# Kernel optimization log

Measured on AMD Instinct MI355X. Metric: run time of the kernel, lower is better.

The kernel has to match this reference:

```python
import jax, jax.numpy as jnp
import numpy as np

B, T, M, P, N2 = 16, 8192, 128, 128, 128  # N2 = N//2 complex modes

def setup_inputs() -> dict:
    key = jax.random.key(0)
    k1, k2, k3, k4, k5 = jax.random.split(key, 5)
    u = jax.random.normal(k1, (B, T, M), dtype=jnp.float32)
    # log-parametrized Lambda (S5 'log' convention): Lambda = -exp(row0) + 1j*row1
    log_re = jnp.log(jax.random.uniform(k2, (N2,), minval=0.1, maxval=1.0))
    im = jnp.pi * jnp.arange(N2, dtype=jnp.float32)  # HiPPO-like imaginary spread
    Lambda_param = jnp.stack([log_re, im], axis=0).astype(jnp.float32)
    B_param = jax.random.normal(k3, (2, N2, M), dtype=jnp.float32) / np.sqrt(M)
    C_param = jax.random.normal(k4, (2, P, N2), dtype=jnp.float32) / np.sqrt(N2)
    delta = jnp.array([0.01], dtype=jnp.float32)  # default_\u0394
    return {"u": u, "Lambda_param": Lambda_param, "B_param": B_param,
            "C_param": C_param, "delta": delta}

def reference(u, Lambda_param, B_param, C_param, delta):
    # Reconstruct complex continuous-time matrices
    Lam = (-jnp.exp(Lambda_param[0]) + 1j * Lambda_param[1]).astype(jnp.complex64)   # (N2,)
    Bc = (B_param[0] + 1j * B_param[1]).astype(jnp.complex64)                        # (N2, M)
    Cc = (C_param[0] + 1j * C_param[1]).astype(jnp.complex64)                        # (P, N2)
    d = delta[0]
    # ZOH discretization: Lambda_d = exp(Lam*d), Bd = ((Lambda_d - 1)/Lam) * B
    Ld = jnp.exp(Lam * d)                                                            # (N2,)
    Bd = ((Ld - 1.0) / Lam)[:, None] * Bc                                            # (N2, M)
    # Input projection: Bu[b,t,n] = sum_m u[b,t,m] * Bd[n,m]
    Bu = jnp.einsum('btm,nm->btn', u.astype(jnp.complex64), Bd)                      # (B,T,N2)
    # Parallel scan of x_{k+1} = Ld * x_k + Bu_k, x_0 = 0 -> x holds x_1..x_T
    A = jnp.broadcast_to(Ld, Bu.shape)
    def comb(e1, e2):
        a1, b1 = e1
        a2, b2 = e2
        return (a1 * a2, a2 * b1 + b2)
    _, x = jax.lax.associative_scan(comb, (A, Bu), axis=1)                           # (B,T,N2)
    # return_next_y=True: y_k = 2*Re(C x_{k+1})
    y = 2.0 * jnp.real(jnp.einsum('btn,pn->btp', x, Cc))                             # (B,T,P)
    return y
```

## Files before the change

### kernel.cpp

```cpp
#include <hip/hip_runtime.h>
#include <hip/hip_bf16.h>

#define LCH 128
#define NCH 64
#define NCHUNKS 1024

typedef __attribute__((ext_vector_type(8))) short short8v;
typedef __attribute__((ext_vector_type(4))) short short4v;
typedef __attribute__((ext_vector_type(4))) float f32x4;

#define W2_LDINV 0
#define W2_LDP   16384
#define W2_E     32768
#define W2_CIN   163840
#define WS_WPACK_BYTE  2359296
#define WS_CCPACK_BYTE (2359296 + 65536)
#define WS_BUS_BYTE    (2359296 + 131072)
#define WS_NEED ((size_t)WS_BUS_BYTE + (size_t)NCHUNKS * 65536)

#define BUS_BYTE(s, np) ((((s) >> 3) * 4096) + ((np) * 16) + (((s) & 7) * 2))

__device__ inline unsigned short f2bf(float f) {
    union { __hip_bfloat16 h; unsigned short u; } v;
    v.h = __float2bfloat16(f);
    return v.u;
}
__device__ inline short4v pack4(float a, float b, float c, float d) {
    union { __hip_bfloat162 h2[2]; short4v s4; } pk;
    pk.h2[0] = __float22bfloat162_rn(make_float2(a, b));
    pk.h2[1] = __float22bfloat162_rn(make_float2(c, d));
    return pk.s4;
}

__global__ void k0_all(const float* __restrict__ lp, const float* __restrict__ bp,
                       const float* __restrict__ cp, const float* __restrict__ delta,
                       float2* __restrict__ ws2, unsigned short* __restrict__ wpack,
                       unsigned short* __restrict__ ccpack) {
    const int r = blockIdx.x;
    const int tid = threadIdx.x;
    if (r < 128) {
        if (tid < 256) {
            const int n = tid & 127;
            const double d = (double)delta[0];
            const double lre = -exp((double)lp[n]);
            const double lim = (double)lp[128 + n];
            const double kk = (double)(r + 1) * d;
            if (tid < 128) {
                const double mag = exp(-lre * kk);
                ws2[W2_LDINV + r * 128 + n] = make_float2((float)(mag * cos(lim * kk)),
                                                          (float)(-mag * sin(lim * kk)));
            } else {
                const double mag = exp(lre * kk);
                ws2[W2_LDP + r * 128 + n] = make_float2((float)(mag * cos(lim * kk)),
                                                        (float)(mag * sin(lim * kk)));
            }
        }
    } else if (r < 192) {
        const int gid = (r - 128) * 512 + tid;
        const int j = gid & 7;
        const int lane = (gid >> 3) & 63;
        const int ks = (gid >> 9) & 3;
        const int ntile = gid >> 11;
        const int np = ntile * 16 + (lane & 15);
        const int m = ks * 32 + ((lane >> 4) & 3) * 8 + j;
        const int n = np & 127;
        const double d = (double)delta[0];
        const double lre = -exp((double)lp[n]);
        const double lim = (double)lp[128 + n];
        const double er = exp(lre * d);
        const double ldr = er * cos(lim * d), ldi = er * sin(lim * d);
        const double nr = ldr - 1.0, ni = ldi;
        const double den = lre * lre + lim * lim;
        const double cr = (nr * lre + ni * lim) / den;
        const double ci = (ni * lre - nr * lim) / den;
        const double br = (double)bp[n * 128 + m];
        const double bi = (double)bp[16384 + n * 128 + m];
        const double v = (np < 128) ? (cr * br - ci * bi) : (cr * bi + ci * br);
        wpack[gid] = f2bf((float)v);
    } else {
        const int gid = (r - 192) * 512 + tid;
        const int j = gid & 7;
        const int lane = (gid >> 3) & 63;
        const int ks = (gid >> 9) & 7;
        const int ptile = gid >> 12;
        const int p = ptile * 16 + (lane & 15);
        const int k = ks * 32 + ((lane >> 4) & 3) * 8 + j;
        const int n = k >> 1;
        const float v = ((k & 1) == 0) ? 2.0f * cp[p * 128 + n]
                                       : -2.0f * cp[16384 + p * 128 + n];
        ccpack[gid] = f2bf(v);
    }
}

__device__ inline void stage_u(const float* __restrict__ uchunk, unsigned short* lds_u) {
    const float4* uf = (const float4*)uchunk;
    const int tid = threadIdx.x;
#pragma unroll
    for (int it = 0; it < 8; ++it) {
        const int f4 = it * 512 + tid;
        const float4 v = uf[f4];
        const int t = f4 >> 5;
        const int m = (f4 & 31) * 4;
        const int byte = (t * 256 + m * 2) ^ ((t & 7) << 4);
        *(short4v*)((char*)lds_u + byte) = pack4(v.x, v.y, v.z, v.w);
    }
}

__global__ __launch_bounds__(512, 4) void k3a_bus(const float* __restrict__ u,
                                                  float2* __restrict__ ws2,
                                                  const unsigned short* __restrict__ wpack,
                                                  char* __restrict__ busg) {
    __shared__ unsigned short lds_u[16384];
    const int tid = threadIdx.x;
    const int lane = tid & 63;
    const int w = tid >> 6;
    const int tl = lane & 15;
    const int gq = (lane >> 4) & 3;
    const int g = blockIdx.x;
    const int b = g >> 6;
    const int c = g & 63;
    const int n = w * 16 + tl;
    const short8v* wp = (const short8v*)wpack;
    char* busc = busg + (size_t)g * 65536;
    const float4* uf = (const float4*)(u + (size_t)(b * 8192 + c * 128) * 128);

    {
        float4 p0 = uf[tid], p1 = uf[512 + tid], p2 = uf[1024 + tid], p3 = uf[1536 + tid];
#pragma unroll
        for (int it = 0; it < 4; ++it) {
            const float4 v = (it == 0) ? p0 : (it == 1) ? p1 : (it == 2) ? p2 : p3;
            const int f4 = it * 512 + tid;
            const int t = f4 >> 5;
            const int m = (f4 & 31) * 4;
            const int byte = (t * 256 + m * 2) ^ ((t & 7) << 4);
            *(short4v*)((char*)lds_u + byte) = pack4(v.x, v.y, v.z, v.w);
        }
    }
    float4 q0 = uf[2048 + tid], q1 = uf[2560 + tid], q2 = uf[3072 + tid], q3 = uf[3584 + tid];
    __builtin_amdgcn_sched_barrier(0);
    __syncthreads();

    float er = 0.f, ei = 0.f;

    {
        f32x4 acc[4][2];
#pragma unroll
        for (int i = 0; i < 4; ++i) { acc[i][0] = (f32x4)0.f; acc[i][1] = (f32x4)0.f; }
        __builtin_amdgcn_s_setprio(1);
#pragma unroll
        for (int ks = 0; ks < 4; ++ks) {
            const short8v b0 = wp[(w * 4 + ks) * 64 + lane];
            const short8v b1 = wp[((8 + w) * 4 + ks) * 64 + lane];
#pragma unroll
            for (int tt2 = 0; tt2 < 4; ++tt2) {
                const int t = tt2 * 16 + tl;
                const int byte = (t * 256 + (ks * 32 + gq * 8) * 2) ^ ((t & 7) << 4);
                const short8v a = *(const short8v*)((const char*)lds_u + byte);
                acc[tt2][0] = __builtin_amdgcn_mfma_f32_16x16x32_bf16(a, b0, acc[tt2][0], 0, 0, 0);
                acc[tt2][1] = __builtin_amdgcn_mfma_f32_16x16x32_bf16(a, b1, acc[tt2][1], 0, 0, 0);
            }
        }
        __builtin_amdgcn_s_setprio(0);
#pragma unroll
        for (int tt2 = 0; tt2 < 4; ++tt2) {
            float vr[4], vi[4];
#pragma unroll
            for (int reg = 0; reg < 4; ++reg) {
                const int rr = tt2 * 16 + gq * 4 + reg;
                const float2 li = ws2[W2_LDINV + rr * 128 + n];
                const float br = acc[tt2][0][reg], bi = acc[tt2][1][reg];
                vr[reg] = li.x * br - li.y * bi;
                vi[reg] = li.x * bi + li.y * br;
                er += vr[reg];
                ei += vi[reg];
            }
            const int s0 = tt2 * 16 + gq * 4;
            const int rowr = w * 16 + tl;
            const int rowi = 128 + rowr;
            *(short4v*)(busc + BUS_BYTE(s0, rowr)) = pack4(vr[0], vr[1], vr[2], vr[3]);
            *(short4v*)(busc + BUS_BYTE(s0, rowi)) = pack4(vi[0], vi[1], vi[2], vi[3]);
        }
    }

    {
#pragma unroll
        for (int it = 0; it < 4; ++it) {
            const float4 v = (it == 0) ? q0 : (it == 1) ? q1 : (it == 2) ? q2 : q3;
            const int f4 = 2048 + it * 512 + tid;
            const int t = f4 >> 5;
            const int m = (f4 & 31) * 4;
            const int byte = (t * 256 + m * 2) ^ ((t & 7) << 4);
            *(short4v*)((char*)lds_u + byte) = pack4(v.x, v.y, v.z, v.w);
        }
    }
    __syncthreads();

    {
        f32x4 acc[4][2];
#pragma unroll
        for (int i = 0; i < 4; ++i) { acc[i][0] = (f32x4)0.f; acc[i][1] = (f32x4)0.f; }
        __builtin_amdgcn_s_setprio(1);
#pragma unroll
        for (int ks = 0; ks < 4; ++ks) {
            const short8v b0 = wp[(w * 4 + ks) * 64 + lane];
            const short8v b1 = wp[((8 + w) * 4 + ks) * 64 + lane];
#pragma unroll
            for (int tt2 = 0; tt2 < 4; ++tt2) {
                const int t = (4 + tt2) * 16 + tl;
                const int byte = (t * 256 + (ks * 32 + gq * 8) * 2) ^ ((t & 7) << 4);
                const short8v a = *(const short8v*)((const char*)lds_u + byte);
                acc[tt2][0] = __builtin_amdgcn_mfma_f32_16x16x32_bf16(a, b0, acc[tt2][0], 0, 0, 0);
                acc[tt2][1] = __builtin_amdgcn_mfma_f32_16x16x32_bf16(a, b1, acc[tt2][1], 0, 0, 0);
            }
        }
        __builtin_amdgcn_s_setprio(0);
#pragma unroll
        for (int tt2 = 0; tt2 < 4; ++tt2) {
            float vr[4], vi[4];
#pragma unroll
            for (int reg = 0; reg < 4; ++reg) {
                const int rr = (4 + tt2) * 16 + gq * 4 + reg;
                const float2 li = ws2[W2_LDINV + rr * 128 + n];
                const float br = acc[tt2][0][reg], bi = acc[tt2][1][reg];
                vr[reg] = li.x * br - li.y * bi;
                vi[reg] = li.x * bi + li.y * br;
                er += vr[reg];
                ei += vi[reg];
            }
            const int s0 = (4 + tt2) * 16 + gq * 4;
            const int rowr = w * 16 + tl;
            const int rowi = 128 + rowr;
            *(short4v*)(busc + BUS_BYTE(s0, rowr)) = pack4(vr[0], vr[1], vr[2], vr[3]);
            *(short4v*)(busc + BUS_BYTE(s0, rowi)) = pack4(vi[0], vi[1], vi[2], vi[3]);
        }
    }

    er += __shfl_xor(er, 16); ei += __shfl_xor(ei, 16);
    er += __shfl_xor(er, 32); ei += __shfl_xor(ei, 32);
    const float2 ld = ws2[W2_LDP + 127 * 128 + n];
    if (lane < 16) {
        ws2[W2_E + g * 128 + n] = make_float2(ld.x * er - ld.y * ei,
                                              ld.x * ei + ld.y * er);
    }
}

__global__ void k2_carry(float2* __restrict__ ws2) {
    const int idx = blockIdx.x * 256 + threadIdx.x;
    const int b = idx >> 7;
    const int n = idx & 127;
    const float2 l = ws2[W2_LDP + 127 * 128 + n];
    float cr = 0.f, ci = 0.f;
    for (int c = 0; c < NCH; ++c) {
        const int o = (b * NCH + c) * 128 + n;
        ws2[W2_CIN + o] = make_float2(cr, ci);
        const float2 e = ws2[W2_E + o];
        const float nr = fmaf(l.x, cr, fmaf(-l.y, ci, e.x));
        const float ni = fmaf(l.x, ci, fmaf(l.y, cr, e.y));
        cr = nr; ci = ni;
    }
}

__global__ __launch_bounds__(512, 6) void k3b_out(const float2* __restrict__ ws2,
                                                  const char* __restrict__ busg,
                                                  const unsigned short* __restrict__ ccpack,
                                                  float* __restrict__ y) {
    __shared__ unsigned short lds[32768];
    const int tid = threadIdx.x;
    const int lane = tid & 63;
    const int w = tid >> 6;
    const int tl = lane & 15;
    const int gq = (lane >> 4) & 3;
    const int g = blockIdx.x;
    const int b = g >> 6;
    const int c = g & 63;
    const int n = w * 16 + tl;
    const short8v* cc8 = (const short8v*)ccpack;
    const char* busc = busg + (size_t)g * 65536;

    short8v ONES, D0, D1;
#pragma unroll
    for (int j = 0; j < 8; ++j) {
        const int sl = gq * 8 + j;
        ONES[j] = (short)0x3F80;
        D0[j] = (sl <= tl) ? (short)0x3F80 : (short)0;
        D1[j] = (sl <= tl + 16) ? (short)0x3F80 : (short)0;
    }
    const float2 cin = ws2[W2_CIN + g * 128 + n];
    const int rowr = w * 16 + tl;
    const int rowi = 128 + rowr;

    {
        f32x4 z[4][2];
#pragma unroll
        for (int i = 0; i < 4; ++i) { z[i][0] = (f32x4)0.f; z[i][1] = (f32x4)0.f; }
        __builtin_amdgcn_s_setprio(1);
#pragma unroll
        for (int ks = 0; ks < 2; ++ks) {
            const int sb = ks * 32 + gq * 8;
            const short8v b0 = *(const short8v*)(busc + BUS_BYTE(sb, rowr));
            const short8v b1 = *(const short8v*)(busc + BUS_BYTE(sb, rowi));
#pragma unroll
            for (int tt = 0; tt < 4; ++tt) {
                if (tt < 2 * ks) continue;
                const short8v a = (tt == 2 * ks) ? D0 : ((tt == 2 * ks + 1) ? D1 : ONES);
                z[tt][0] = __builtin_amdgcn_mfma_f32_16x16x32_bf16(a, b0, z[tt][0], 0, 0, 0);
                z[tt][1] = __builtin_amdgcn_mfma_f32_16x16x32_bf16(a, b1, z[tt][1], 0, 0, 0);
            }
        }
        __builtin_amdgcn_s_setprio(0);
#pragma unroll
        for (int tt = 0; tt < 4; ++tt) {
#pragma unroll
            for (int reg = 0; reg < 4; ++reg) {
                const int r = tt * 16 + gq * 4 + reg;
                const float2 ld = ws2[W2_LDP + r * 128 + n];
                const float zr = z[tt][0][reg] + cin.x;
                const float zi = z[tt][1][reg] + cin.y;
                const float xr = ld.x * zr - ld.y * zi;
                const float xi = ld.x * zi + ld.y * zr;
                union { __hip_bfloat162 h2; unsigned uu; } pk;
                pk.h2 = __float22bfloat162_rn(make_float2(xr, xi));
                const int byte = (r * 512 + n * 4) ^ ((r & 7) << 4);
                *(unsigned*)((char*)lds + byte) = pk.uu;
            }
        }
    }

    {
        f32x4 z[4][2];
#pragma unroll
        for (int i = 0; i < 4; ++i) { z[i][0] = (f32x4)0.f; z[i][1] = (f32x4)0.f; }
        __builtin_amdgcn_s_setprio(1);
#pragma unroll
        for (int ks = 0; ks < 4; ++ks) {
            const int sb = ks * 32 + gq * 8;
            const short8v b0 = *(const short8v*)(busc + BUS_BYTE(sb, rowr));
            const short8v b1 = *(const short8v*)(busc + BUS_BYTE(sb, rowi));
#pragma unroll
            for (int tt2 = 0; tt2 < 4; ++tt2) {
                const int tt = 4 + tt2;
                if (tt < 2 * ks) continue;
                const short8v a = (tt == 2 * ks) ? D0 : ((tt == 2 * ks + 1) ? D1 : ONES);
                z[tt2][0] = __builtin_amdgcn_mfma_f32_16x16x32_bf16(a, b0, z[tt2][0], 0, 0, 0);
                z[tt2][1] = __builtin_amdgcn_mfma_f32_16x16x32_bf16(a, b1, z[tt2][1], 0, 0, 0);
            }
        }
        __builtin_amdgcn_s_setprio(0);
#pragma unroll
        for (int tt2 = 0; tt2 < 4; ++tt2) {
#pragma unroll
            for (int reg = 0; reg < 4; ++reg) {
                const int r = (4 + tt2) * 16 + gq * 4 + reg;
                const float2 ld = ws2[W2_LDP + r * 128 + n];
                const float zr = z[tt2][0][reg] + cin.x;
                const float zi = z[tt2][1][reg] + cin.y;
                const float xr = ld.x * zr - ld.y * zi;
                const float xi = ld.x * zi + ld.y * zr;
                union { __hip_bfloat162 h2; unsigned uu; } pk;
                pk.h2 = __float22bfloat162_rn(make_float2(xr, xi));
                const int byte = (r * 512 + n * 4) ^ ((r & 7) << 4);
                *(unsigned*)((char*)lds + byte) = pk.uu;
            }
        }
    }
    __syncthreads();

    f32x4 yac[8];
#pragma unroll
    for (int i = 0; i < 8; ++i) yac[i] = (f32x4)0.f;
    __builtin_amdgcn_s_setprio(1);
#pragma unroll
    for (int ks = 0; ks < 8; ++ks) {
        const short8v bfrg = cc8[(w * 8 + ks) * 64 + lane];
#pragma unroll
        for (int tt = 0; tt < 8; ++tt) {
            const int t = tt * 16 + tl;
            const int byte = (t * 512 + (ks * 32 + gq * 8) * 2) ^ ((t & 7) << 4);
            const short8v a = *(const short8v*)((const char*)lds + byte);
            yac[tt] = __builtin_amdgcn_mfma_f32_16x16x32_bf16(a, bfrg, yac[tt], 0, 0, 0);
        }
    }
    __builtin_amdgcn_s_setprio(0);
    const int p = w * 16 + tl;
    float* yrow = y + (size_t)(b * 8192 + c * 128) * 128;
#pragma unroll
    for (int tt = 0; tt < 8; ++tt) {
#pragma unroll
        for (int reg = 0; reg < 4; ++reg) {
            const int t = tt * 16 + gq * 4 + reg;
            yrow[t * 128 + p] = yac[tt][reg];
        }
    }
}

__global__ __launch_bounds__(512, 4) void k1_end(const float* __restrict__ u,
                                                 float2* __restrict__ ws2,
                                                 const unsigned short* __restrict__ wpack) {
    __shared__ unsigned short lds_u[16384];
    const int tid = threadIdx.x;
    const int lane = tid & 63;
    const int w = tid >> 6;
    const int tl = lane & 15;
    const int gq = (lane >> 4) & 3;
    const int g = blockIdx.x;
    const int b = g >> 6;
    const int c = g & 63;
    const int n = w * 16 + tl;
    stage_u(u + (size_t)(b * 8192 + c * 128) * 128, lds_u);
    __syncthreads();
    const short8v* wp = (const short8v*)wpack;
    float er = 0.f, ei = 0.f;
#pragma unroll
    for (int h = 0; h < 2; ++h) {
        f32x4 acc[4][2];
#pragma unroll
        for (int i = 0; i < 4; ++i) { acc[i][0] = (f32x4)0.f; acc[i][1] = (f32x4)0.f; }
        __builtin_amdgcn_s_setprio(1);
#pragma unroll
        for (int ks = 0; ks < 4; ++ks) {
            const short8v b0 = wp[(w * 4 + ks) * 64 + lane];
            const short8v b1 = wp[((8 + w) * 4 + ks) * 64 + lane];
#pragma unroll
            for (int tt2 = 0; tt2 < 4; ++tt2) {
                const int t = (h * 4 + tt2) * 16 + tl;
                const int byte = (t * 256 + (ks * 32 + gq * 8) * 2) ^ ((t & 7) << 4);
                const short8v a = *(const short8v*)((const char*)lds_u + byte);
                acc[tt2][0] = __builtin_amdgcn_mfma_f32_16x16x32_bf16(a, b0, acc[tt2][0], 0, 0, 0);
                acc[tt2][1] = __builtin_amdgcn_mfma_f32_16x16x32_bf16(a, b1, acc[tt2][1], 0, 0, 0);
            }
        }
        __builtin_amdgcn_s_setprio(0);
        __builtin_amdgcn_sched_barrier(0);
#pragma unroll
        for (int tt2 = 0; tt2 < 4; ++tt2) {
#pragma unroll
            for (int reg = 0; reg < 4; ++reg) {
                const int r = (h * 4 + tt2) * 16 + gq * 4 + reg;
                const float2 li = ws2[W2_LDINV + r * 128 + n];
                const float br = acc[tt2][0][reg], bi = acc[tt2][1][reg];
                er += li.x * br - li.y * bi;
                ei += li.x * bi + li.y * br;
            }
        }
        __builtin_amdgcn_sched_barrier(0);
    }
    er += __shfl_xor(er, 16); ei += __shfl_xor(ei, 16);
    er += __shfl_xor(er, 32); ei += __shfl_xor(ei, 32);
    const float2 ld = ws2[W2_LDP + 127 * 128 + n];
    if (lane < 16) {
        ws2[W2_E + g * 128 + n] = make_float2(ld.x * er - ld.y * ei,
                                              ld.x * ei + ld.y * er);
    }
}

__global__ __launch_bounds__(512, 4) void k3_main(const float* __restrict__ u,
                                                  const float2* __restrict__ ws2,
                                                  const unsigned short* __restrict__ wpack,
                                                  const unsigned short* __restrict__ ccpack,
                                                  float* __restrict__ y) {
    __shared__ unsigned short lds[32768];
    const int tid = threadIdx.x;
    const int lane = tid & 63;
    const int w = tid >> 6;
    const int tl = lane & 15;
    const int gq = (lane >> 4) & 3;
    const int g = blockIdx.x;
    const int b = g >> 6;
    const int c = g & 63;
    const int n = w * 16 + tl;
    const short8v* wp = (const short8v*)wpack;
    const short8v* cc8 = (const short8v*)ccpack;

    stage_u(u + (size_t)(b * 8192 + c * 128) * 128, lds);
    __syncthreads();
#pragma unroll
    for (int hh = 0; hh < 2; ++hh) {
        const int h = 1 - hh;
        f32x4 acc[4][2];
#pragma unroll
        for (int i = 0; i < 4; ++i) { acc[i][0] = (f32x4)0.f; acc[i][1] = (f32x4)0.f; }
        __builtin_amdgcn_s_setprio(1);
#pragma unroll
        for (int ks = 0; ks < 4; ++ks) {
            const short8v b0 = wp[(w * 4 + ks) * 64 + lane];
            const short8v b1 = wp[((8 + w) * 4 + ks) * 64 + lane];
#pragma unroll
            for (int tt2 = 0; tt2 < 4; ++tt2) {
                const int t = (h * 4 + tt2) * 16 + tl;
                const int byte = (t * 256 + (ks * 32 + gq * 8) * 2) ^ ((t & 7) << 4);
                const short8v a = *(const short8v*)((const char*)lds + byte);
                acc[tt2][0] = __builtin_amdgcn_mfma_f32_16x16x32_bf16(a, b0, acc[tt2][0], 0, 0, 0);
                acc[tt2][1] = __builtin_amdgcn_mfma_f32_16x16x32_bf16(a, b1, acc[tt2][1], 0, 0, 0);
            }
        }
        __builtin_amdgcn_s_setprio(0);
        __builtin_amdgcn_sched_barrier(0);
        if (h == 0) __syncthreads();
#pragma unroll
        for (int tt2 = 0; tt2 < 4; ++tt2) {
            float vr[4], vi[4];
#pragma unroll
            for (int reg = 0; reg < 4; ++reg) {
                const int r = (h * 4 + tt2) * 16 + gq * 4 + reg;
                const float2 li = ws2[W2_LDINV + r * 128 + n];
                const float br = acc[tt2][0][reg], bi = acc[tt2][1][reg];
                vr[reg] = li.x * br - li.y * bi;
                vi[reg] = li.x * bi + li.y * br;
            }
            const int s0 = (h * 4 + tt2) * 16 + gq * 4;
            const int rowr = w * 16 + tl;
            const int rowi = 128 + rowr;
            *(short4v*)((char*)lds + BUS_BYTE(s0, rowr)) = pack4(vr[0], vr[1], vr[2], vr[3]);
            *(short4v*)((char*)lds + BUS_BYTE(s0, rowi)) = pack4(vi[0], vi[1], vi[2], vi[3]);
        }
        __builtin_amdgcn_sched_barrier(0);
    }
    short8v ONES, D0, D1;
#pragma unroll
    for (int j = 0; j < 8; ++j) {
        const int sl = gq * 8 + j;
        ONES[j] = (short)0x3F80;
        D0[j] = (sl <= tl) ? (short)0x3F80 : (short)0;
        D1[j] = (sl <= tl + 16) ? (short)0x3F80 : (short)0;
    }
    f32x4 z[8][2];
#pragma unroll
    for (int i = 0; i < 8; ++i) { z[i][0] = (f32x4)0.f; z[i][1] = (f32x4)0.f; }
#pragma unroll
    for (int ks = 0; ks < 4; ++ks) {
        const int sb = ks * 32 + gq * 8;
        const int rowr = w * 16 + tl;
        const int rowi = 128 + rowr;
        const short8v b0 = *(const short8v*)((const char*)lds + BUS_BYTE(sb, rowr));
        const short8v b1 = *(const short8v*)((const char*)lds + BUS_BYTE(sb, rowi));
#pragma unroll
        for (int tt = 0; tt < 8; ++tt) {
            if (tt < 2 * ks) continue;
            const short8v a = (tt == 2 * ks) ? D0 : ((tt == 2 * ks + 1) ? D1 : ONES);
            z[tt][0] = __builtin_amdgcn_mfma_f32_16x16x32_bf16(a, b0, z[tt][0], 0, 0, 0);
            z[tt][1] = __builtin_amdgcn_mfma_f32_16x16x32_bf16(a, b1, z[tt][1], 0, 0, 0);
        }
    }
    __syncthreads();
    const float2 cin = ws2[W2_CIN + g * 128 + n];
#pragma unroll
    for (int tt = 0; tt < 8; ++tt) {
#pragma unroll
        for (int reg = 0; reg < 4; ++reg) {
            const int r = tt * 16 + gq * 4 + reg;
            const float2 ld = ws2[W2_LDP + r * 128 + n];
            const float zr = z[tt][0][reg] + cin.x;
            const float zi = z[tt][1][reg] + cin.y;
            const float xr = ld.x * zr - ld.y * zi;
            const float xi = ld.x * zi + ld.y * zr;
            union { __hip_bfloat162 h2; unsigned uu; } pk;
            pk.h2 = __float22bfloat162_rn(make_float2(xr, xi));
            const int byte = (r * 512 + n * 4) ^ ((r & 7) << 4);
            *(unsigned*)((char*)lds + byte) = pk.uu;
        }
    }
    __syncthreads();
    f32x4 yac[8];
#pragma unroll
    for (int i = 0; i < 8; ++i) yac[i] = (f32x4)0.f;
    __builtin_amdgcn_s_setprio(1);
#pragma unroll
    for (int ks = 0; ks < 8; ++ks) {
        const short8v bfrg = cc8[(w * 8 + ks) * 64 + lane];
#pragma unroll
        for (int tt = 0; tt < 8; ++tt) {
            const int t = tt * 16 + tl;
            const int byte = (t * 512 + (ks * 32 + gq * 8) * 2) ^ ((t & 7) << 4);
            const short8v a = *(const short8v*)((const char*)lds + byte);
            yac[tt] = __builtin_amdgcn_mfma_f32_16x16x32_bf16(a, bfrg, yac[tt], 0, 0, 0);
        }
    }
    __builtin_amdgcn_s_setprio(0);
    const int p = w * 16 + tl;
    float* yrow = y + (size_t)(b * 8192 + c * 128) * 128;
#pragma unroll
    for (int tt = 0; tt < 8; ++tt) {
#pragma unroll
        for (int reg = 0; reg < 4; ++reg) {
            const int t = tt * 16 + gq * 4 + reg;
            yrow[t * 128 + p] = yac[tt][reg];
        }
    }
}

extern "C" void kernel_launch(void* const* d_in, const int* in_sizes, int n_in,
                              void* d_out, int out_size, void* d_ws, size_t ws_size,
                              hipStream_t stream) {
    const float* u     = (const float*)d_in[0];
    const float* lp    = (const float*)d_in[1];
    const float* bp    = (const float*)d_in[2];
    const float* cp    = (const float*)d_in[3];
    const float* delta = (const float*)d_in[4];
    float* y  = (float*)d_out;
    float2* ws2 = (float2*)d_ws;
    unsigned short* wpack  = (unsigned short*)((char*)d_ws + WS_WPACK_BYTE);
    unsigned short* ccpack = (unsigned short*)((char*)d_ws + WS_CCPACK_BYTE);
    char* busg = (char*)d_ws + WS_BUS_BYTE;

    k0_all<<<256, 512, 0, stream>>>(lp, bp, cp, delta, ws2, wpack, ccpack);

    if (ws_size >= WS_NEED) {
        k3a_bus <<<NCHUNKS, 512, 0, stream>>>(u, ws2, wpack, busg);
        k2_carry<<<8, 256, 0, stream>>>(ws2);
        k3b_out <<<NCHUNKS, 512, 0, stream>>>(ws2, busg, ccpack, y);
    } else {
        k1_end  <<<NCHUNKS, 512, 0, stream>>>(u, ws2, wpack);
        k2_carry<<<8, 256, 0, stream>>>(ws2);
        k3_main <<<NCHUNKS, 512, 0, stream>>>(u, ws2, wpack, ccpack, y);
    }
}
```

Baseline: 81.73 us.

## Stage Bu output through LDS for coalesced stores and raise occupancy bound

The k3a_bus kernel now processes the 128-step chunk as two 64-row halves in a loop. Each half stages only 16KB of u in LDS. The bf16 Bu tile is written into a 32KB LDS region first, then copied to global with contiguous float4 stores instead of scattered short4 stores. The register prefetch of the second u half is dropped, and the launch-bounds occupancy hint rises from 4 to 6. This trades the earlier load/compute overlap and adds an extra LDS round trip and barriers, in exchange for coalesced global writes and tighter register limits.

```diff
diff --git a/kernel.cpp b/kernel.cpp
--- a/kernel.cpp
+++ b/kernel.cpp
@@ -106,11 +106,11 @@
     }
 }
 
-__global__ __launch_bounds__(512, 4) void k3a_bus(const float* __restrict__ u,
+__global__ __launch_bounds__(512, 6) void k3a_bus(const float* __restrict__ u,
                                                   float2* __restrict__ ws2,
                                                   const unsigned short* __restrict__ wpack,
                                                   char* __restrict__ busg) {
-    __shared__ unsigned short lds_u[16384];
+    __shared__ unsigned short lds[24576];
     const int tid = threadIdx.x;
     const int lane = tid & 63;
     const int w = tid >> 6;
@@ -124,25 +124,23 @@
     char* busc = busg + (size_t)g * 65536;
     const float4* uf = (const float4*)(u + (size_t)(b * 8192 + c * 128) * 128);
 
-    {
-        float4 p0 = uf[tid], p1 = uf[512 + tid], p2 = uf[1024 + tid], p3 = uf[1536 + tid];
+    float er = 0.f, ei = 0.f;
+    const int rowr = w * 16 + tl;
+    const int rowi = 128 + rowr;
+
+#pragma unroll
+    for (int h = 0; h < 2; ++h) {
 #pragma unroll
         for (int it = 0; it < 4; ++it) {
-            const float4 v = (it == 0) ? p0 : (it == 1) ? p1 : (it == 2) ? p2 : p3;
-            const int f4 = it * 512 + tid;
-            const int t = f4 >> 5;
-            const int m = (f4 & 31) * 4;
+            const int f4l = it * 512 + tid;
+            const float4 v = uf[h * 2048 + f4l];
+            const int t = f4l >> 5;
+            const int m = (f4l & 31) * 4;
             const int byte = (t * 256 + m * 2) ^ ((t & 7) << 4);
-            *(short4v*)((char*)lds_u + byte) = pack4(v.x, v.y, v.z, v.w);
-        }
-    }
-    float4 q0 = uf[2048 + tid], q1 = uf[2560 + tid], q2 = uf[3072 + tid], q3 = uf[3584 + tid];
-    __builtin_amdgcn_sched_barrier(0);
-    __syncthreads();
-
-    float er = 0.f, ei = 0.f;
-
-    {
+            *(short4v*)((char*)lds + byte) = pack4(v.x, v.y, v.z, v.w);
+        }
+        __syncthreads();
+
         f32x4 acc[4][2];
 #pragma unroll
         for (int i = 0; i < 4; ++i) { acc[i][0] = (f32x4)0.f; acc[i][1] = (f32x4)0.f; }
@@ -155,18 +153,19 @@
             for (int tt2 = 0; tt2 < 4; ++tt2) {
                 const int t = tt2 * 16 + tl;
                 const int byte = (t * 256 + (ks * 32 + gq * 8) * 2) ^ ((t & 7) << 4);
-                const short8v a = *(const short8v*)((const char*)lds_u + byte);
+                const short8v a = *(const short8v*)((const char*)lds + byte);
                 acc[tt2][0] = __builtin_amdgcn_mfma_f32_16x16x32_bf16(a, b0, acc[tt2][0], 0, 0, 0);
                 acc[tt2][1] = __builtin_amdgcn_mfma_f32_16x16x32_bf16(a, b1, acc[tt2][1], 0, 0, 0);
             }
         }
         __builtin_amdgcn_s_setprio(0);
+
 #pragma unroll
         for (int tt2 = 0; tt2 < 4; ++tt2) {
             float vr[4], vi[4];
 #pragma unroll
             for (int reg = 0; reg < 4; ++reg) {
-                const int rr = tt2 * 16 + gq * 4 + reg;
+                const int rr = h * 64 + tt2 * 16 + gq * 4 + reg;
                 const float2 li = ws2[W2_LDINV + rr * 128 + n];
                 const float br = acc[tt2][0][reg], bi = acc[tt2][1][reg];
                 vr[reg] = li.x * br - li.y * bi;
@@ -175,63 +174,20 @@
                 ei += vi[reg];
             }
             const int s0 = tt2 * 16 + gq * 4;
-            const int rowr = w * 16 + tl;
-            const int rowi = 128 + rowr;
-            *(short4v*)(busc + BUS_BYTE(s0, rowr)) = pack4(vr[0], vr[1], vr[2], vr[3]);
-            *(short4v*)(busc + BUS_BYTE(s0, rowi)) = pack4(vi[0], vi[1], vi[2], vi[3]);
-        }
-    }
-
-    {
-#pragma unroll
-        for (int it = 0; it < 4; ++it) {
-            const float4 v = (it == 0) ? q0 : (it == 1) ? q1 : (it == 2) ? q2 : q3;
-            const int f4 = 2048 + it * 512 + tid;
-            const int t = f4 >> 5;
-            const int m = (f4 & 31) * 4;
-            const int byte = (t * 256 + m * 2) ^ ((t & 7) << 4);
-            *(short4v*)((char*)lds_u + byte) = pack4(v.x, v.y, v.z, v.w);
-        }
-    }
-    __syncthreads();
-
-    {
-        f32x4 acc[4][2];
-#pragma unroll
-        for (int i = 0; i < 4; ++i) { acc[i][0] = (f32x4)0.f; acc[i][1] = (f32x4)0.f; }
-        __builtin_amdgcn_s_setprio(1);
-#pragma unroll
-        for (int ks = 0; ks < 4; ++ks) {
-            const short8v b0 = wp[(w * 4 + ks) * 64 + lane];
-            const short8v b1 = wp[((8 + w) * 4 + ks) * 64 + lane];
-#pragma unroll
-            for (int tt2 = 0; tt2 < 4; ++tt2) {
-                const int t = (4 + tt2) * 16 + tl;
-                const int byte = (t * 256 + (ks * 32 + gq * 8) * 2) ^ ((t & 7) << 4);
-                const short8v a = *(const short8v*)((const char*)lds_u + byte);
-                acc[tt2][0] = __builtin_amdgcn_mfma_f32_16x16x32_bf16(a, b0, acc[tt2][0], 0, 0, 0);
-                acc[tt2][1] = __builtin_amdgcn_mfma_f32_16x16x32_bf16(a, b1, acc[tt2][1], 0, 0, 0);
-            }
-        }
-        __builtin_amdgcn_s_setprio(0);
-#pragma unroll
-        for (int tt2 = 0; tt2 < 4; ++tt2) {
-            float vr[4], vi[4];
-#pragma unroll
-            for (int reg = 0; reg < 4; ++reg) {
-                const int rr = (4 + tt2) * 16 + gq * 4 + reg;
-                const float2 li = ws2[W2_LDINV + rr * 128 + n];
-                const float br = acc[tt2][0][reg], bi = acc[tt2][1][reg];
-                vr[reg] = li.x * br - li.y * bi;
-                vi[reg] = li.x * bi + li.y * br;
-                er += vr[reg];
-                ei += vi[reg];
-            }
-            const int s0 = (4 + tt2) * 16 + gq * 4;
-            const int rowr = w * 16 + tl;
-            const int rowi = 128 + rowr;
-            *(short4v*)(busc + BUS_BYTE(s0, rowr)) = pack4(vr[0], vr[1], vr[2], vr[3]);
-            *(short4v*)(busc + BUS_BYTE(s0, rowi)) = pack4(vi[0], vi[1], vi[2], vi[3]);
+            *(short4v*)((char*)lds + 16384 + BUS_BYTE(s0, rowr)) =
+                pack4(vr[0], vr[1], vr[2], vr[3]);
+            *(short4v*)((char*)lds + 16384 + BUS_BYTE(s0, rowi)) =
+                pack4(vi[0], vi[1], vi[2], vi[3]);
+        }
+        __syncthreads();
+
+        {
+            const float4* src = (const float4*)((const char*)lds + 16384);
+            float4* dst = (float4*)(busc + h * 32768);
+#pragma unroll
+            for (int it = 0; it < 4; ++it) {
+                dst[it * 512 + tid] = src[it * 512 + tid];
+            }
         }
     }
 
```

After: 92.03 us. 1.13x slower.

## Split output projection into two halves to halve LDS footprint

Applied to the files above, without the earlier changes.

The output kernel now computes the C projection and stores y for the first 64 timesteps before building the state tile for the second 64 timesteps, reusing a 32 KB LDS buffer instead of 64 KB. This halves shared memory per block and the yac accumulator count, which may allow more resident blocks and overlap of the y stores with the second half's work. Stores of y switch to nontemporal. The cost is an extra barrier pair and reloading the C fragments twice.

```diff
diff --git a/kernel.cpp b/kernel.cpp
--- a/kernel.cpp
+++ b/kernel.cpp
@@ -264,7 +264,7 @@
                                                   const char* __restrict__ busg,
                                                   const unsigned short* __restrict__ ccpack,
                                                   float* __restrict__ y) {
-    __shared__ unsigned short lds[32768];
+    __shared__ unsigned short lds[16384];
     const int tid = threadIdx.x;
     const int lane = tid & 63;
     const int w = tid >> 6;
@@ -276,6 +276,8 @@
     const int n = w * 16 + tl;
     const short8v* cc8 = (const short8v*)ccpack;
     const char* busc = busg + (size_t)g * 65536;
+    float* yrow = y + (size_t)(b * 8192 + c * 128) * 128;
+    const int p = w * 16 + tl;
 
     short8v ONES, D0, D1;
 #pragma unroll
@@ -325,6 +327,34 @@
             }
         }
     }
+    __syncthreads();
+    {
+        f32x4 yac[4];
+#pragma unroll
+        for (int i = 0; i < 4; ++i) yac[i] = (f32x4)0.f;
+        __builtin_amdgcn_s_setprio(1);
+#pragma unroll
+        for (int ks = 0; ks < 8; ++ks) {
+            const short8v bfrg = cc8[(w * 8 + ks) * 64 + lane];
+#pragma unroll
+            for (int tt = 0; tt < 4; ++tt) {
+                const int t = tt * 16 + tl;
+                const int byte = (t * 512 + (ks * 32 + gq * 8) * 2) ^ ((t & 7) << 4);
+                const short8v a = *(const short8v*)((const char*)lds + byte);
+                yac[tt] = __builtin_amdgcn_mfma_f32_16x16x32_bf16(a, bfrg, yac[tt], 0, 0, 0);
+            }
+        }
+        __builtin_amdgcn_s_setprio(0);
+#pragma unroll
+        for (int tt = 0; tt < 4; ++tt) {
+#pragma unroll
+            for (int reg = 0; reg < 4; ++reg) {
+                const int t = tt * 16 + gq * 4 + reg;
+                __builtin_nontemporal_store(yac[tt][reg], &yrow[t * 128 + p]);
+            }
+        }
+    }
+    __syncthreads();
 
     {
         f32x4 z[4][2];
@@ -351,6 +381,7 @@
 #pragma unroll
             for (int reg = 0; reg < 4; ++reg) {
                 const int r = (4 + tt2) * 16 + gq * 4 + reg;
+                const int rl = r - 64;
                 const float2 ld = ws2[W2_LDP + r * 128 + n];
                 const float zr = z[tt2][0][reg] + cin.x;
                 const float zi = z[tt2][1][reg] + cin.y;
@@ -358,37 +389,36 @@
                 const float xi = ld.x * zi + ld.y * zr;
                 union { __hip_bfloat162 h2; unsigned uu; } pk;
                 pk.h2 = __float22bfloat162_rn(make_float2(xr, xi));
-                const int byte = (r * 512 + n * 4) ^ ((r & 7) << 4);
+                const int byte = (rl * 512 + n * 4) ^ ((rl & 7) << 4);
                 *(unsigned*)((char*)lds + byte) = pk.uu;
             }
         }
     }
     __syncthreads();
-
-    f32x4 yac[8];
-#pragma unroll
-    for (int i = 0; i < 8; ++i) yac[i] = (f32x4)0.f;
-    __builtin_amdgcn_s_setprio(1);
-#pragma unroll
-    for (int ks = 0; ks < 8; ++ks) {
-        const short8v bfrg = cc8[(w * 8 + ks) * 64 + lane];
-#pragma unroll
-        for (int tt = 0; tt < 8; ++tt) {
-            const int t = tt * 16 + tl;
-            const int byte = (t * 512 + (ks * 32 + gq * 8) * 2) ^ ((t & 7) << 4);
-            const short8v a = *(const short8v*)((const char*)lds + byte);
-            yac[tt] = __builtin_amdgcn_mfma_f32_16x16x32_bf16(a, bfrg, yac[tt], 0, 0, 0);
-        }
-    }
-    __builtin_amdgcn_s_setprio(0);
-    const int p = w * 16 + tl;
-    float* yrow = y + (size_t)(b * 8192 + c * 128) * 128;
-#pragma unroll
-    for (int tt = 0; tt < 8; ++tt) {
-#pragma unroll
-        for (int reg = 0; reg < 4; ++reg) {
-            const int t = tt * 16 + gq * 4 + reg;
-            yrow[t * 128 + p] = yac[tt][reg];
+    {
+        f32x4 yac[4];
+#pragma unroll
+        for (int i = 0; i < 4; ++i) yac[i] = (f32x4)0.f;
+        __builtin_amdgcn_s_setprio(1);
+#pragma unroll
+        for (int ks = 0; ks < 8; ++ks) {
+            const short8v bfrg = cc8[(w * 8 + ks) * 64 + lane];
+#pragma unroll
+            for (int tt2 = 0; tt2 < 4; ++tt2) {
+                const int tloc = tt2 * 16 + tl;
+                const int byte = (tloc * 512 + (ks * 32 + gq * 8) * 2) ^ ((tloc & 7) << 4);
+                const short8v a = *(const short8v*)((const char*)lds + byte);
+                yac[tt2] = __builtin_amdgcn_mfma_f32_16x16x32_bf16(a, bfrg, yac[tt2], 0, 0, 0);
+            }
+        }
+        __builtin_amdgcn_s_setprio(0);
+#pragma unroll
+        for (int tt2 = 0; tt2 < 4; ++tt2) {
+#pragma unroll
+            for (int reg = 0; reg < 4; ++reg) {
+                const int t = (4 + tt2) * 16 + gq * 4 + reg;
+                __builtin_nontemporal_store(yac[tt2][reg], &yrow[t * 128 + p]);
+            }
         }
     }
 }
```

New measurement: 127.7 us. +56.2%, slower.
